# Performance work log

Hardware: AMD Instinct MI355X
Metric: run time of the kernel (lower is better)

The kernel has to match this reference:

```python
import jax, jax.numpy as jnp
import numpy as np

B, L, D = 2, 512, 1024
INNER = 32
PAIR = 128


def setup_inputs() -> dict:
    key = jax.random.key(0)
    ks = jax.random.split(key, 6)
    scale = lambda fan_in: 1.0 / np.sqrt(fan_in)
    return {
        "sequence_state": jax.random.normal(ks[0], (B, L, D), dtype=jnp.float32),
        "ln_gamma": jnp.ones((D,), dtype=jnp.float32),
        "ln_beta": jnp.zeros((D,), dtype=jnp.float32),
        "W_proj": jax.random.normal(ks[1], (2 * INNER, D), dtype=jnp.float32) * scale(D),
        "b_proj": jnp.zeros((2 * INNER,), dtype=jnp.float32),
        "W_o": jax.random.normal(ks[2], (PAIR, 2 * INNER), dtype=jnp.float32) * scale(2 * INNER),
        "b_o": jnp.zeros((PAIR,), dtype=jnp.float32),
    }


def reference(sequence_state, ln_gamma, ln_beta, W_proj, b_proj, W_o, b_o):
    eps = 1e-5
    # LayerNorm over last dim
    mu = jnp.mean(sequence_state, axis=-1, keepdims=True)
    var = jnp.mean(jnp.square(sequence_state - mu), axis=-1, keepdims=True)
    s = (sequence_state - mu) * jax.lax.rsqrt(var + eps) * ln_gamma + ln_beta
    # proj: B x L x 2*inner
    s = jnp.einsum("bld,ed->ble", s, W_proj) + b_proj
    q, k = jnp.split(s, 2, axis=-1)  # each B x L x inner
    # broadcast outer product / difference: B x L x L x inner
    prod = q[:, None, :, :] * k[:, :, None, :]
    diff = q[:, None, :, :] - k[:, :, None, :]
    x = jnp.concatenate([prod, diff], axis=-1)  # B x L x L x 2*inner
    # o_proj: B x L x L x pairwise
    x = jnp.einsum("bije,pe->bijp", x, W_o) + b_o
    return x
```

## Files before the change

### kernel.cpp

```cpp
#include <hip/hip_runtime.h>
#include <hip/hip_bf16.h>
#include <stdint.h>


typedef __attribute__((ext_vector_type(8))) short short8;
typedef __attribute__((ext_vector_type(4))) float floatx4;

__device__ __forceinline__ unsigned short f2bf(float f) {
    union { float f; unsigned int u; } v; v.f = f;
    return (unsigned short)((v.u + 0x7FFFu + ((v.u >> 16) & 1u)) >> 16);
}

__device__ __forceinline__ floatx4 fmadd4(float s, floatx4 w, floatx4 a) {
    a.x += s * w.x; a.y += s * w.y; a.z += s * w.z; a.w += s * w.w; return a;
}

__global__ __launch_bounds__(256) void k0_transpose(
    const float* __restrict__ Wproj, const float* __restrict__ Wo,
    float* __restrict__ Wt, float* __restrict__ Wot, float* __restrict__ Wdt)
{
    int g = blockIdx.x * 256 + threadIdx.x;
    if (g < 65536) {
        int o = g >> 10, d = g & 1023;
        Wt[d * 64 + o] = Wproj[g];
    } else {
        int h = g - 65536;
        int p = h & 127, e = h >> 7;
        float v = Wo[p * 64 + e];
        if (e < 32) Wot[e * 128 + p] = v;
        else        Wdt[(e - 32) * 128 + p] = v;
    }
}

__global__ __launch_bounds__(256) void k1_ln_proj(
    const float* __restrict__ x, const float* __restrict__ gamma, const float* __restrict__ beta,
    const float* __restrict__ Wt, const float* __restrict__ b_proj,
    const float* __restrict__ Wdt, const float* __restrict__ b_o,
    unsigned short* __restrict__ Qbf, float* __restrict__ Kf, float* __restrict__ C0)
{
    __shared__ __attribute__((aligned(16))) float s_sh[4][1024];
    __shared__ __attribute__((aligned(16))) float part[4][16][68];
    __shared__ float k_sh[4][32];

    const int t = threadIdx.x;
    const int w = t >> 6;
    const int lane = t & 63;
    const int row = blockIdx.x * 4 + w;

    const float* xr = x + (size_t)row * 1024;
    floatx4 xv[4];
    float sum = 0.f, sq = 0.f;
#pragma unroll
    for (int c = 0; c < 4; ++c) {
        xv[c] = *(const floatx4*)(xr + (c * 64 + lane) * 4);
        sum += xv[c].x + xv[c].y + xv[c].z + xv[c].w;
        sq  += xv[c].x * xv[c].x + xv[c].y * xv[c].y + xv[c].z * xv[c].z + xv[c].w * xv[c].w;
    }
#pragma unroll
    for (int m = 1; m < 64; m <<= 1) {
        sum += __shfl_xor(sum, m, 64);
        sq  += __shfl_xor(sq,  m, 64);
    }
    const float mu   = sum * (1.f / 1024.f);
    const float var  = sq * (1.f / 1024.f) - mu * mu;
    const float rsig = rsqrtf(var + 1e-5f);
#pragma unroll
    for (int c = 0; c < 4; ++c) {
        int d = (c * 64 + lane) * 4;
        floatx4 g4 = *(const floatx4*)(gamma + d);
        floatx4 b4 = *(const floatx4*)(beta + d);
        floatx4 s4;
        s4.x = (xv[c].x - mu) * rsig * g4.x + b4.x;
        s4.y = (xv[c].y - mu) * rsig * g4.y + b4.y;
        s4.z = (xv[c].z - mu) * rsig * g4.z + b4.z;
        s4.w = (xv[c].w - mu) * rsig * g4.w + b4.w;
        *(floatx4*)(&s_sh[w][d]) = s4;
    }
    __syncthreads();

    {
        const int o4 = t & 15;
        const int ch = t >> 4;
        const floatx4* Wt4 = (const floatx4*)Wt;
        floatx4 a0 = {0.f, 0.f, 0.f, 0.f}, a1 = a0, a2 = a0, a3 = a0;
        const int dbase = ch * 64;
#pragma unroll 8
        for (int dd = 0; dd < 64; ++dd) {
            const int d = dbase + dd;
            floatx4 w4 = Wt4[d * 16 + o4];
            a0 = fmadd4(s_sh[0][d], w4, a0);
            a1 = fmadd4(s_sh[1][d], w4, a1);
            a2 = fmadd4(s_sh[2][d], w4, a2);
            a3 = fmadd4(s_sh[3][d], w4, a3);
        }
        *(floatx4*)&part[0][ch][o4 * 4] = a0;
        *(floatx4*)&part[1][ch][o4 * 4] = a1;
        *(floatx4*)&part[2][ch][o4 * 4] = a2;
        *(floatx4*)&part[3][ch][o4 * 4] = a3;
    }
    __syncthreads();

    {
        const int r = t >> 6, oo = t & 63;
        float v = b_proj[oo];
#pragma unroll
        for (int c = 0; c < 16; ++c) v += part[r][c][oo];
        const int rowr = blockIdx.x * 4 + r;
        if (oo < 32) {
            Qbf[rowr * 32 + oo] = f2bf(v);
        } else {
            Kf[rowr * 32 + (oo - 32)] = v;
            k_sh[r][oo - 32] = v;
        }
    }
    __syncthreads();

    {
        const int p = t & 127;
        const int r0 = t >> 7;
#pragma unroll
        for (int rr = 0; rr < 2; ++rr) {
            const int r = r0 * 2 + rr;
            float a = 0.f;
#pragma unroll 8
            for (int e = 0; e < 32; ++e) a += k_sh[r][e] * Wdt[e * 128 + p];
            C0[(size_t)(blockIdx.x * 4 + r) * 128 + p] = b_o[p] - a;
        }
    }
}

__global__ __launch_bounds__(256) void k2_pair(
    const unsigned short* __restrict__ Qbf, const float* __restrict__ Kf,
    const float* __restrict__ C0, const float* __restrict__ Wot, const float* __restrict__ Wdt,
    float* __restrict__ out)
{
    __shared__ unsigned short G[32 * 136];
    __shared__ __attribute__((aligned(16))) float T[4][16][132];
    __shared__ float c0s[128];
    __shared__ float ksh[32];

    const int t    = threadIdx.x;
    const int bi   = blockIdx.x >> 1;
    const int half = blockIdx.x & 1;
    const int b    = bi >> 9;

    if (t < 32)  ksh[t] = Kf[(size_t)bi * 32 + t];
    if (t < 128) c0s[t] = C0[(size_t)bi * 128 + t];
    __syncthreads();

#pragma unroll
    for (int it = 0; it < 16; ++it) {
        int idx = it * 256 + t;
        int e = idx >> 7, p = idx & 127;
        float gv = ksh[e] * Wot[idx] + Wdt[idx];
        G[e * 136 + p] = f2bf(gv);
    }
    __syncthreads();

    const int wave = t >> 6, lane = t & 63;
    const int col = lane & 15, quad = lane >> 4;

    short8 bfrag[8];
#pragma unroll
    for (int pt = 0; pt < 8; ++pt) {
        short8 f;
#pragma unroll
        for (int u = 0; u < 8; ++u)
            f[u] = (short)G[(quad * 8 + u) * 136 + pt * 16 + col];
        bfrag[pt] = f;
    }
    float cv[8];
#pragma unroll
    for (int pt = 0; pt < 8; ++pt) cv[pt] = c0s[pt * 16 + col];

    const size_t outbase = (size_t)bi * (512 * 128);
    float (*Tw)[132] = T[wave];

    for (int l = 0; l < 4; ++l) {
        const int jt = half * 16 + wave * 4 + l;
        const int j0 = jt * 16;
        const short8 afrag =
            *(const short8*)(Qbf + ((size_t)b * 512 + j0 + col) * 32 + quad * 8);
        floatx4 acc[8];
#pragma unroll
        for (int pt = 0; pt < 8; ++pt) {
            floatx4 c;
            c.x = cv[pt]; c.y = cv[pt]; c.z = cv[pt]; c.w = cv[pt];
            acc[pt] = __builtin_amdgcn_mfma_f32_16x16x32_bf16(afrag, bfrag[pt], c, 0, 0, 0);
        }
#pragma unroll
        for (int pt = 0; pt < 8; ++pt) {
#pragma unroll
            for (int r = 0; r < 4; ++r)
                Tw[quad * 4 + r][pt * 16 + col] = acc[pt][r];
        }
        float* orow = out + outbase + (size_t)j0 * 128;
#pragma unroll
        for (int s = 0; s < 8; ++s) {
            int idx = s * 64 + lane;
            int rr = idx >> 5, c4 = idx & 31;
            floatx4 v = *(const floatx4*)&Tw[rr][c4 * 4];
            __builtin_nontemporal_store(v, (floatx4*)(orow + rr * 128 + c4 * 4));
        }
    }
}

extern "C" void kernel_launch(void* const* d_in, const int* in_sizes, int n_in,
                              void* d_out, int out_size, void* d_ws, size_t ws_size,
                              hipStream_t stream) {
    const float* x     = (const float*)d_in[0];
    const float* gamma = (const float*)d_in[1];
    const float* beta  = (const float*)d_in[2];
    const float* Wproj = (const float*)d_in[3];
    const float* bproj = (const float*)d_in[4];
    const float* Wo    = (const float*)d_in[5];
    const float* bo    = (const float*)d_in[6];
    float* out = (float*)d_out;

    float* ws = (float*)d_ws;
    float* Wt  = ws;
    float* Wot = ws + 65536;
    float* Wdt = ws + 69632;
    float* Kf  = ws + 73728;
    float* C0  = ws + 106496;
    unsigned short* Qbf = (unsigned short*)(ws + 237568);

    hipLaunchKernelGGL(k0_transpose, dim3(288), dim3(256), 0, stream,
                       Wproj, Wo, Wt, Wot, Wdt);
    hipLaunchKernelGGL(k1_ln_proj, dim3(256), dim3(256), 0, stream,
                       x, gamma, beta, Wt, bproj, Wdt, bo, Qbf, Kf, C0);
    hipLaunchKernelGGL(k2_pair, dim3(2048), dim3(256), 0, stream,
                       Qbf, Kf, C0, Wot, Wdt, out);
}
```

Before: 284.8 us.

## Swap MFMA operands so output stores directly without LDS transpose

```diff
diff --git a/kernel.cpp b/kernel.cpp
--- a/kernel.cpp
+++ b/kernel.cpp
@@ -17,7 +17,7 @@
 
 __global__ __launch_bounds__(256) void k0_transpose(
     const float* __restrict__ Wproj, const float* __restrict__ Wo,
-    float* __restrict__ Wt, float* __restrict__ Wot, float* __restrict__ Wdt)
+    float* __restrict__ Wt, float* __restrict__ Wdt)
 {
     int g = blockIdx.x * 256 + threadIdx.x;
     if (g < 65536) {
@@ -26,9 +26,7 @@
     } else {
         int h = g - 65536;
         int p = h & 127, e = h >> 7;
-        float v = Wo[p * 64 + e];
-        if (e < 32) Wot[e * 128 + p] = v;
-        else        Wdt[(e - 32) * 128 + p] = v;
+        Wdt[e * 128 + p] = Wo[p * 64 + 32 + e];
     }
 }
 
@@ -131,12 +129,11 @@
 
 __global__ __launch_bounds__(256) void k2_pair(
     const unsigned short* __restrict__ Qbf, const float* __restrict__ Kf,
-    const float* __restrict__ C0, const float* __restrict__ Wot, const float* __restrict__ Wdt,
+    const float* __restrict__ C0, const float* __restrict__ Wo,
     float* __restrict__ out)
 {
-    __shared__ unsigned short G[32 * 136];
-    __shared__ __attribute__((aligned(16))) float T[4][16][132];
-    __shared__ float c0s[128];
+    __shared__ __attribute__((aligned(16))) unsigned short Gt[128 * 32];
+    __shared__ __attribute__((aligned(16))) float c0s[128];
     __shared__ float ksh[32];
 
     const int t    = threadIdx.x;
@@ -151,57 +148,40 @@
 #pragma unroll
     for (int it = 0; it < 16; ++it) {
         int idx = it * 256 + t;
-        int e = idx >> 7, p = idx & 127;
-        float gv = ksh[e] * Wot[idx] + Wdt[idx];
-        G[e * 136 + p] = f2bf(gv);
+        int p = idx >> 5, e = idx & 31;
+        float gv = ksh[e] * Wo[p * 64 + e] + Wo[p * 64 + 32 + e];
+        Gt[p * 32 + e] = f2bf(gv);
     }
     __syncthreads();
 
     const int wave = t >> 6, lane = t & 63;
     const int col = lane & 15, quad = lane >> 4;
 
-    short8 bfrag[8];
-#pragma unroll
-    for (int pt = 0; pt < 8; ++pt) {
-        short8 f;
-#pragma unroll
-        for (int u = 0; u < 8; ++u)
-            f[u] = (short)G[(quad * 8 + u) * 136 + pt * 16 + col];
-        bfrag[pt] = f;
-    }
-    float cv[8];
-#pragma unroll
-    for (int pt = 0; pt < 8; ++pt) cv[pt] = c0s[pt * 16 + col];
+    short8 gfrag[8];
+#pragma unroll
+    for (int pt = 0; pt < 8; ++pt)
+        gfrag[pt] = *(const short8*)&Gt[(pt * 16 + col) * 32 + quad * 8];
+
+    floatx4 cinit[8];
+#pragma unroll
+    for (int pt = 0; pt < 8; ++pt)
+        cinit[pt] = *(const floatx4*)&c0s[pt * 16 + quad * 4];
 
     const size_t outbase = (size_t)bi * (512 * 128);
-    float (*Tw)[132] = T[wave];
+    const unsigned short* qbase = Qbf + (size_t)b * 512 * 32;
 
     for (int l = 0; l < 4; ++l) {
         const int jt = half * 16 + wave * 4 + l;
         const int j0 = jt * 16;
-        const short8 afrag =
-            *(const short8*)(Qbf + ((size_t)b * 512 + j0 + col) * 32 + quad * 8);
+        const short8 qfrag = *(const short8*)(qbase + (size_t)(j0 + col) * 32 + quad * 8);
         floatx4 acc[8];
 #pragma unroll
-        for (int pt = 0; pt < 8; ++pt) {
-            floatx4 c;
-            c.x = cv[pt]; c.y = cv[pt]; c.z = cv[pt]; c.w = cv[pt];
-            acc[pt] = __builtin_amdgcn_mfma_f32_16x16x32_bf16(afrag, bfrag[pt], c, 0, 0, 0);
-        }
-#pragma unroll
-        for (int pt = 0; pt < 8; ++pt) {
-#pragma unroll
-            for (int r = 0; r < 4; ++r)
-                Tw[quad * 4 + r][pt * 16 + col] = acc[pt][r];
-        }
-        float* orow = out + outbase + (size_t)j0 * 128;
-#pragma unroll
-        for (int s = 0; s < 8; ++s) {
-            int idx = s * 64 + lane;
-            int rr = idx >> 5, c4 = idx & 31;
-            floatx4 v = *(const floatx4*)&Tw[rr][c4 * 4];
-            __builtin_nontemporal_store(v, (floatx4*)(orow + rr * 128 + c4 * 4));
-        }
+        for (int pt = 0; pt < 8; ++pt)
+            acc[pt] = __builtin_amdgcn_mfma_f32_16x16x32_bf16(gfrag[pt], qfrag, cinit[pt], 0, 0, 0);
+        float* op = out + outbase + (size_t)(j0 + col) * 128 + quad * 4;
+#pragma unroll
+        for (int pt = 0; pt < 8; ++pt)
+            __builtin_nontemporal_store(acc[pt], (floatx4*)(op + pt * 16));
     }
 }
 
@@ -219,16 +199,15 @@
 
     float* ws = (float*)d_ws;
     float* Wt  = ws;
-    float* Wot = ws + 65536;
-    float* Wdt = ws + 69632;
-    float* Kf  = ws + 73728;
-    float* C0  = ws + 106496;
-    unsigned short* Qbf = (unsigned short*)(ws + 237568);
-
-    hipLaunchKernelGGL(k0_transpose, dim3(288), dim3(256), 0, stream,
-                       Wproj, Wo, Wt, Wot, Wdt);
+    float* Wdt = ws + 65536;
+    float* Kf  = ws + 69632;
+    float* C0  = ws + 102400;
+    unsigned short* Qbf = (unsigned short*)(ws + 233472);
+
+    hipLaunchKernelGGL(k0_transpose, dim3(272), dim3(256), 0, stream,
+                       Wproj, Wo, Wt, Wdt);
     hipLaunchKernelGGL(k1_ln_proj, dim3(256), dim3(256), 0, stream,
                        x, gamma, beta, Wt, bproj, Wdt, bo, Qbf, Kf, C0);
     hipLaunchKernelGGL(k2_pair, dim3(2048), dim3(256), 0, stream,
-                       Qbf, Kf, C0, Wot, Wdt, out);
-}
+                       Qbf, Kf, C0, Wo, out);
+}
```

Result: slower. 329.1 us (+15.6%).
